# Optimization experiments

Measured on AMD Instinct MI355X. Metric: run time of the kernel, lower is better.

Reference implementation:

```python
import jax, jax.numpy as jnp
import numpy as np

BS, T, F, D_IN, NH, D_OUT = 8, 32, 128, 64, 8, 64
GAUSS_STD = 2.0


def setup_inputs() -> dict:
    key = jax.random.key(0)
    ks = jax.random.split(key, 9)
    X = jax.random.normal(ks[0], (BS, F, T, D_IN), dtype=jnp.float32)
    W_query = jax.random.normal(ks[1], (T, F, D_IN, NH, 2), dtype=jnp.float32)
    W_key = jax.random.normal(ks[2], (T, F, D_IN, NH, 2), dtype=jnp.float32)
    Wkey_ = jax.random.normal(ks[3], (T, 2, 2), dtype=jnp.float32)
    u = jax.random.normal(ks[4], (T, F, 2), dtype=jnp.float32)
    attention_center = GAUSS_STD * jax.random.normal(ks[5], (T, NH, 1), dtype=jnp.float32)
    alpha = jax.random.normal(ks[6], (T,), dtype=jnp.float32)
    # relative position features: [F, F, 2] = (delta^2, delta), tiled over T
    rel = (jnp.arange(F)[None, :] - jnp.arange(F)[:, None]).astype(jnp.float32)
    R = jnp.broadcast_to(jnp.stack([rel ** 2, rel], axis=-1)[None], (T, F, F, 2))
    W = jax.random.normal(ks[7], (T, NH * D_IN, D_OUT), dtype=jnp.float32)
    b = jax.random.normal(ks[8], (F, T, D_OUT), dtype=jnp.float32)
    return {"X": X, "W_query": W_query, "W_key": W_key, "Wkey_": Wkey_,
            "u": u, "attention_center": attention_center, "alpha": alpha,
            "R": R, "W": W, "b": b}


def reference(X, W_query, W_key, Wkey_, u, attention_center, alpha, R, W, b):
    # X: [bs, F, T, d_in] -> [bs, T, F, d_in]
    Xp = jnp.transpose(X, (0, 2, 1, 3))
    bs = Xp.shape[0]
    query = jnp.einsum('btfd,tfdhe->btfhe', Xp, W_query)  # [bs,T,F,Nh,2]
    key_t = jnp.einsum('btfd,tfdhe->btfhe', Xp, W_key)    # [bs,T,F,Nh,2]
    r_delta = jnp.einsum('tde,tfle->tfld', Wkey_, R)      # [T,F,F,2]
    centers = jnp.concatenate([jnp.ones_like(attention_center),
                               -2.0 * attention_center], axis=-1)  # [T,Nh,2]
    v = -alpha[:, None, None] * centers                   # [T,Nh,2]
    scores = (jnp.einsum('btfhe,btlhe->btfhl', query, key_t)
              + jnp.einsum('btfhe,tfle->btfhl', query, r_delta)
              + jnp.einsum('tle,btfhe->btfhl', u, key_t)
              + jnp.einsum('the,tfle->tfhl', v, r_delta)[None])  # [bs,T,F,Nh,F]
    probs = jax.nn.softmax(scores, axis=-1)
    vals = jnp.einsum('btfhl,btld->btfhd', probs, Xp)     # [bs,T,F,Nh,d_in]
    vals = vals.reshape(bs, T, F, NH * D_IN)
    out = jnp.einsum('btfd,tdo->bfto', vals, W) + b[None]  # [bs,F,T,d_out]
    return out
```

## Files before the change

### kernel.cpp

```cpp
#include <hip/hip_runtime.h>
#include <hip/hip_bf16.h>

#define NBS 8
#define NT 32
#define NF 128
#define NDIN 64
#define NNH 8
#define NDOUT 64

typedef __bf16 bf16_t;
typedef __bf16 bf16x8 __attribute__((ext_vector_type(8)));
typedef float f32x4 __attribute__((ext_vector_type(4)));
typedef float f32x2 __attribute__((ext_vector_type(2)));

__global__ __launch_bounds__(256, 4)
void qk_project_kernel(const float* __restrict__ X,
                       const float* __restrict__ Wq,
                       const float* __restrict__ Wk,
                       float* __restrict__ q_ws,
                       float* __restrict__ k_ws)
{
    __shared__ float lx[4][8][64];
    const int w = threadIdx.x >> 6, lane = threadIdx.x & 63;
    const int gw = blockIdx.x * 4 + w;
    const int t = gw >> 7, f = gw & 127;

    {
        const int b = lane >> 3, d8 = (lane & 7) << 3;
        const float* src = &X[(((size_t)b * NF + f) * NT + t) * NDIN + d8];
        const float4 v0 = *(const float4*)src;
        const float4 v1 = *(const float4*)(src + 4);
        *(float4*)&lx[w][b][d8]     = v0;
        *(float4*)&lx[w][b][d8 + 4] = v1;
    }
    __syncthreads();

    const int dq = lane >> 4, he = lane & 15;
    const float* wq = Wq + ((size_t)t * NF + f) * (NDIN * 16);
    const float* wk = Wk + ((size_t)t * NF + f) * (NDIN * 16);
    float qa[8] = {0,0,0,0,0,0,0,0}, ka[8] = {0,0,0,0,0,0,0,0};
    for (int d0 = 0; d0 < NDIN; d0 += 4) {
        const int d = d0 + dq;
        const float wqv = wq[d * 16 + he];
        const float wkv = wk[d * 16 + he];
#pragma unroll
        for (int b = 0; b < 8; ++b) {
            const float x = lx[w][b][d];
            qa[b] = fmaf(x, wqv, qa[b]);
            ka[b] = fmaf(x, wkv, ka[b]);
        }
    }
#pragma unroll
    for (int b = 0; b < 8; ++b) {
        qa[b] += __shfl_xor(qa[b], 16); qa[b] += __shfl_xor(qa[b], 32);
        ka[b] += __shfl_xor(ka[b], 16); ka[b] += __shfl_xor(ka[b], 32);
    }
#pragma unroll
    for (int bb = 0; bb < 2; ++bb) {
        const int b = dq + bb * 4;
        q_ws[(((size_t)b * NT + t) * 16 + he) * NF + f] = qa[b];
        k_ws[(((size_t)b * NT + t) * 16 + he) * NF + f] = ka[b];
    }
}

__global__ __launch_bounds__(512, 2)
void spatial_attn_kernel(const float* __restrict__ X,
                         const float* __restrict__ q_ws,
                         const float* __restrict__ k_ws,
                         const float* __restrict__ Wkey,
                         const float* __restrict__ U,
                         const float* __restrict__ AC,
                         const float* __restrict__ Alpha,
                         const float* __restrict__ Wo,
                         const float* __restrict__ Bias,
                         float* __restrict__ Out)
{
    const int blk  = blockIdx.x;
    const int b    = blk & 7;
    const int t    = blk >> 3;
    const int tid  = threadIdx.x;
    const int w    = tid >> 6;
    const int lane = tid & 63;
    const int cq   = lane & 15;
    const int rq   = lane >> 4;
    const int rt   = w;
    const int frow = 16 * rt + cq;

    __shared__ __align__(16) unsigned char smem[140288];
    bf16_t* XTs   = (bf16_t*)smem;
    float*  kvf   = (float*)(smem + 16384);
    float4 (*qf)[128] = (float4 (*)[128])(smem + 40960);
    bf16_t* WTall = (bf16_t*)(smem + 57344);
    bf16_t (*Vscr)[16][68] = (bf16_t (*)[16][68])(smem + 122880);

#pragma unroll
    for (int r = 0; r < 4; ++r) {
        const int idx = tid + r * 512;
        const int f = idx >> 4, d4 = (idx & 15) << 2;
        const float4 v = *(const float4*)&X[(((size_t)b * NF + f) * NT + t) * NDIN + d4];
        float vv[4]; vv[0] = v.x; vv[1] = v.y; vv[2] = v.z; vv[3] = v.w;
#pragma unroll
        for (int i = 0; i < 4; ++i) {
            const int d = d4 + i;
            XTs[d * 128 + (((f >> 3) ^ (d & 15)) << 3) + (f & 7)] = (bf16_t)vv[i];
        }
    }
#pragma unroll
    for (int r = 0; r < 2; ++r) {
        const int idx = tid + r * 512;
        const int hh = idx >> 7, l = idx & 127;
        const size_t qkb = ((size_t)b * NT + t) * 16;
        const float k0 = k_ws[(qkb + 2 * hh + 0) * NF + l];
        const float k1 = k_ws[(qkb + 2 * hh + 1) * NF + l];
        const float q0 = q_ws[(qkb + 2 * hh + 0) * NF + l];
        const float q1 = q_ws[(qkb + 2 * hh + 1) * NF + l];
        const float2 u01 = *(const float2*)&U[((size_t)t * NF + l) * 2];
        qf[hh][l] = make_float4(q0, q1, k0, k1);
        const int P = l >> 1, c = l & 1;
        const int base = (hh * 64 + P) * 12;
        kvf[base + 0 + c] = k0;
        kvf[base + 2 + c] = k1;
        kvf[base + 4 + c] = u01.x;
        kvf[base + 6 + c] = u01.y;
    }
#pragma unroll
    for (int rep = 0; rep < 16; ++rep) {
        const int flat = rep * 512 + tid;
        const int h = flat >> 10, f10 = flat & 1023;
        const int dd = f10 >> 4, o4 = (f10 & 15) << 2;
        const float4 v = *(const float4*)&Wo[((size_t)t * 512 + h * 64 + dd) * NDOUT + o4];
        float vv[4]; vv[0] = v.x; vv[1] = v.y; vv[2] = v.z; vv[3] = v.w;
#pragma unroll
        for (int i = 0; i < 4; ++i) {
            const int o = o4 + i;
            WTall[h * 4096 + o * 64 + (((dd >> 3) ^ (o & 7)) << 3) + (dd & 7)] = (bf16_t)vv[i];
        }
    }

    const float alpha_t = Alpha[t];
    const float wk00 = Wkey[t * 4 + 0], wk01 = Wkey[t * 4 + 1];
    const float wk10 = Wkey[t * 4 + 2], wk11 = Wkey[t * 4 + 3];

    __syncthreads();

    f32x4 oacc[4] = { {0.f,0.f,0.f,0.f}, {0.f,0.f,0.f,0.f}, {0.f,0.f,0.f,0.f}, {0.f,0.f,0.f,0.f} };

#pragma unroll 1
    for (int h = 0; h < NNH; ++h) {
        const float4 qq = qf[h][frow];
        const float q0 = qq.x, q1 = qq.y, kf0 = qq.z, kf1 = qq.w;
        const float v1 = 2.f * alpha_t * AC[t * NNH + h];
        const float c0 = (q0 - alpha_t) * wk00 + (q1 + v1) * wk10;
        const float c1 = (q0 - alpha_t) * wk01 + (q1 + v1) * wk11;

        f32x2 sc2[4][4];
        f32x2 mx2 = { -3.0e38f, -3.0e38f };
#pragma unroll
        for (int kt = 0; kt < 4; ++kt) {
#pragma unroll
            for (int j2 = 0; j2 < 4; ++j2) {
                const int P = kt * 16 + rq * 4 + j2;
                const float4 ld0 = *(const float4*)&kvf[(h * 64 + P) * 12];
                const float4 ld1 = *(const float4*)&kvf[(h * 64 + P) * 12 + 4];
                const f32x2 k0p = { ld0.x, ld0.y };
                const f32x2 k1p = { ld0.z, ld0.w };
                const f32x2 u0p = { ld1.x, ld1.y };
                const f32x2 u1p = { ld1.z, ld1.w };
                const float l0 = (float)(kt * 32 + rq * 8 + 2 * j2 - frow);
                const f32x2 delp = { l0, l0 + 1.f };
                f32x2 sv = k0p * q0 + k1p * q1 + u0p * kf0 + u1p * kf1
                         + (delp * c0 + c1) * delp;
                sc2[kt][j2] = sv;
                mx2 = __builtin_elementwise_max(mx2, sv);
            }
        }
        float rowmax = fmaxf(mx2.x, mx2.y);
        rowmax = fmaxf(rowmax, __shfl_xor(rowmax, 16));
        rowmax = fmaxf(rowmax, __shfl_xor(rowmax, 32));
        f32x2 s2 = { 0.f, 0.f };
#pragma unroll
        for (int kt = 0; kt < 4; ++kt)
#pragma unroll
            for (int j2 = 0; j2 < 4; ++j2) {
                f32x2 sv = sc2[kt][j2];
                const f32x2 e = { __expf(sv.x - rowmax), __expf(sv.y - rowmax) };
                s2 += e;
                sc2[kt][j2] = e;
            }
        float sum = s2.x + s2.y;
        sum += __shfl_xor(sum, 16);
        sum += __shfl_xor(sum, 32);
        const float rinv = 1.f / sum;

        f32x4 vacc[4] = { {0.f,0.f,0.f,0.f}, {0.f,0.f,0.f,0.f}, {0.f,0.f,0.f,0.f}, {0.f,0.f,0.f,0.f} };
#pragma unroll
        for (int kt = 0; kt < 4; ++kt) {
            bf16x8 pf;
#pragma unroll
            for (int j2 = 0; j2 < 4; ++j2) {
                const f32x2 e = sc2[kt][j2];
                pf[2 * j2 + 0] = (bf16_t)(e.x * rinv);
                pf[2 * j2 + 1] = (bf16_t)(e.y * rinv);
            }
#pragma unroll
            for (int ct = 0; ct < 4; ++ct) {
                const bf16x8 bb = *(const bf16x8*)&XTs[(ct * 16 + cq) * 128 + (((kt * 4 + rq) ^ cq) << 3)];
                vacc[ct] = __builtin_amdgcn_mfma_f32_16x16x32_bf16(pf, bb, vacc[ct], 0, 0, 0);
            }
        }
#pragma unroll
        for (int ct = 0; ct < 4; ++ct)
#pragma unroll
            for (int rr = 0; rr < 4; ++rr)
                Vscr[w][rq * 4 + rr][ct * 16 + cq] = (bf16_t)vacc[ct][rr];

#pragma unroll
        for (int kt = 0; kt < 2; ++kt) {
            const bf16x8 a = *(const bf16x8*)&Vscr[w][cq][kt * 32 + rq * 8];
#pragma unroll
            for (int ct = 0; ct < 4; ++ct) {
                const bf16x8 bw = *(const bf16x8*)&WTall[h * 4096 + (ct * 16 + cq) * 64 + (((kt * 4 + rq) ^ (cq & 7)) << 3)];
                oacc[ct] = __builtin_amdgcn_mfma_f32_16x16x32_bf16(a, bw, oacc[ct], 0, 0, 0);
            }
        }
    }

#pragma unroll
    for (int ct = 0; ct < 4; ++ct) {
#pragma unroll
        for (int rr = 0; rr < 4; ++rr) {
            const int f = 16 * rt + rq * 4 + rr;
            const int o = ct * 16 + cq;
            Out[(((size_t)b * NF + f) * NT + t) * NDOUT + o] =
                oacc[ct][rr] + Bias[((size_t)f * NT + t) * NDOUT + o];
        }
    }
}

extern "C" void kernel_launch(void* const* d_in, const int* in_sizes, int n_in,
                              void* d_out, int out_size, void* d_ws, size_t ws_size,
                              hipStream_t stream) {
    (void)in_sizes; (void)n_in; (void)ws_size; (void)out_size;
    const float* X    = (const float*)d_in[0];
    const float* Wq   = (const float*)d_in[1];
    const float* Wk   = (const float*)d_in[2];
    const float* Wkey = (const float*)d_in[3];
    const float* U    = (const float*)d_in[4];
    const float* AC   = (const float*)d_in[5];
    const float* Al   = (const float*)d_in[6];
    const float* Wo   = (const float*)d_in[8];
    const float* Bias = (const float*)d_in[9];

    float* q_ws = (float*)d_ws;
    float* k_ws = q_ws + (size_t)NBS * NT * 16 * NF;

    qk_project_kernel<<<dim3(NT * NF / 4), dim3(256), 0, stream>>>(X, Wq, Wk, q_ws, k_ws);
    spatial_attn_kernel<<<dim3(NBS * NT), dim3(512), 0, stream>>>(
        X, q_ws, k_ws, Wkey, U, AC, Al, Wo, Bias, (float*)d_out);
}
```

Before: 49.01 us.

## Double-buffer per-head output weights and deduplicate u in LDS to shrink shared memory

Shared memory per block drops from about 140KB to about 76KB. Instead of staging all eight heads of the output projection weights at once, the kernel keeps a two-slot buffer and loads the next head's weights inside the head loop. The u positional terms are stored once rather than copied for every head. The aim is to fit more blocks per CU and overlap the weight loads with compute, at the cost of a __syncthreads every iteration and global loads inside the loop.

Measured after the change: 52.24 us. +6.6%, slower.

```diff
diff --git a/kernel.cpp b/kernel.cpp
--- a/kernel.cpp
+++ b/kernel.cpp
@@ -86,12 +86,13 @@
     const int rt   = w;
     const int frow = 16 * rt + cq;
 
-    __shared__ __align__(16) unsigned char smem[140288];
+    __shared__ __align__(16) unsigned char smem[75776];
     bf16_t* XTs   = (bf16_t*)smem;
-    float*  kvf   = (float*)(smem + 16384);
-    float4 (*qf)[128] = (float4 (*)[128])(smem + 40960);
-    bf16_t* WTall = (bf16_t*)(smem + 57344);
-    bf16_t (*Vscr)[16][68] = (bf16_t (*)[16][68])(smem + 122880);
+    float*  kvh   = (float*)(smem + 16384);
+    float*  kvu   = (float*)(smem + 24576);
+    float4 (*qf)[128] = (float4 (*)[128])(smem + 25600);
+    bf16_t* WTs   = (bf16_t*)(smem + 41984);
+    bf16_t (*Vscr)[16][68] = (bf16_t (*)[16][68])(smem + 58368);
 
 #pragma unroll
     for (int r = 0; r < 4; ++r) {
@@ -114,26 +115,29 @@
         const float k1 = k_ws[(qkb + 2 * hh + 1) * NF + l];
         const float q0 = q_ws[(qkb + 2 * hh + 0) * NF + l];
         const float q1 = q_ws[(qkb + 2 * hh + 1) * NF + l];
-        const float2 u01 = *(const float2*)&U[((size_t)t * NF + l) * 2];
         qf[hh][l] = make_float4(q0, q1, k0, k1);
         const int P = l >> 1, c = l & 1;
-        const int base = (hh * 64 + P) * 12;
-        kvf[base + 0 + c] = k0;
-        kvf[base + 2 + c] = k1;
-        kvf[base + 4 + c] = u01.x;
-        kvf[base + 6 + c] = u01.y;
-    }
-#pragma unroll
-    for (int rep = 0; rep < 16; ++rep) {
-        const int flat = rep * 512 + tid;
-        const int h = flat >> 10, f10 = flat & 1023;
-        const int dd = f10 >> 4, o4 = (f10 & 15) << 2;
-        const float4 v = *(const float4*)&Wo[((size_t)t * 512 + h * 64 + dd) * NDOUT + o4];
+        const int base = (hh * 64 + P) * 4;
+        kvh[base + 0 + c] = k0;
+        kvh[base + 2 + c] = k1;
+    }
+    if (tid < 128) {
+        const int l = tid;
+        const float2 u01 = *(const float2*)&U[((size_t)t * NF + l) * 2];
+        const int P = l >> 1, c = l & 1;
+        kvu[P * 4 + 0 + c] = u01.x;
+        kvu[P * 4 + 2 + c] = u01.y;
+    }
+#pragma unroll
+    for (int r = 0; r < 2; ++r) {
+        const int idx = tid + r * 512;
+        const int dd = idx >> 4, o4 = (idx & 15) << 2;
+        const float4 v = *(const float4*)&Wo[((size_t)t * 512 + dd) * NDOUT + o4];
         float vv[4]; vv[0] = v.x; vv[1] = v.y; vv[2] = v.z; vv[3] = v.w;
 #pragma unroll
         for (int i = 0; i < 4; ++i) {
             const int o = o4 + i;
-            WTall[h * 4096 + o * 64 + (((dd >> 3) ^ (o & 7)) << 3) + (dd & 7)] = (bf16_t)vv[i];
+            WTs[o * 64 + (((dd >> 3) ^ (o & 7)) << 3) + (dd & 7)] = (bf16_t)vv[i];
         }
     }
 
@@ -147,6 +151,22 @@
 
 #pragma unroll 1
     for (int h = 0; h < NNH; ++h) {
+        if (h < 7) {
+            const int bn = ((h + 1) & 1) * 4096;
+#pragma unroll
+            for (int r = 0; r < 2; ++r) {
+                const int idx = tid + r * 512;
+                const int dd = idx >> 4, o4 = (idx & 15) << 2;
+                const float4 v = *(const float4*)&Wo[((size_t)t * 512 + (h + 1) * 64 + dd) * NDOUT + o4];
+                float vv[4]; vv[0] = v.x; vv[1] = v.y; vv[2] = v.z; vv[3] = v.w;
+#pragma unroll
+                for (int i = 0; i < 4; ++i) {
+                    const int o = o4 + i;
+                    WTs[bn + o * 64 + (((dd >> 3) ^ (o & 7)) << 3) + (dd & 7)] = (bf16_t)vv[i];
+                }
+            }
+        }
+        const int buf = (h & 1) * 4096;
         const float4 qq = qf[h][frow];
         const float q0 = qq.x, q1 = qq.y, kf0 = qq.z, kf1 = qq.w;
         const float v1 = 2.f * alpha_t * AC[t * NNH + h];
@@ -160,12 +180,12 @@
 #pragma unroll
             for (int j2 = 0; j2 < 4; ++j2) {
                 const int P = kt * 16 + rq * 4 + j2;
-                const float4 ld0 = *(const float4*)&kvf[(h * 64 + P) * 12];
-                const float4 ld1 = *(const float4*)&kvf[(h * 64 + P) * 12 + 4];
-                const f32x2 k0p = { ld0.x, ld0.y };
-                const f32x2 k1p = { ld0.z, ld0.w };
-                const f32x2 u0p = { ld1.x, ld1.y };
-                const f32x2 u1p = { ld1.z, ld1.w };
+                const float4 kp = *(const float4*)&kvh[(h * 64 + P) * 4];
+                const float4 up = *(const float4*)&kvu[P * 4];
+                const f32x2 k0p = { kp.x, kp.y };
+                const f32x2 k1p = { kp.z, kp.w };
+                const f32x2 u0p = { up.x, up.y };
+                const f32x2 u1p = { up.z, up.w };
                 const float l0 = (float)(kt * 32 + rq * 8 + 2 * j2 - frow);
                 const f32x2 delp = { l0, l0 + 1.f };
                 f32x2 sv = k0p * q0 + k1p * q1 + u0p * kf0 + u1p * kf1
@@ -219,10 +239,11 @@
             const bf16x8 a = *(const bf16x8*)&Vscr[w][cq][kt * 32 + rq * 8];
 #pragma unroll
             for (int ct = 0; ct < 4; ++ct) {
-                const bf16x8 bw = *(const bf16x8*)&WTall[h * 4096 + (ct * 16 + cq) * 64 + (((kt * 4 + rq) ^ (cq & 7)) << 3)];
+                const bf16x8 bw = *(const bf16x8*)&WTs[buf + (ct * 16 + cq) * 64 + (((kt * 4 + rq) ^ (cq & 7)) << 3)];
                 oacc[ct] = __builtin_amdgcn_mfma_f32_16x16x32_bf16(a, bw, oacc[ct], 0, 0, 0);
             }
         }
+        __syncthreads();
     }
 
 #pragma unroll
```

## Software-pipeline softmax of next head with MFMA GEMMs of current head

Applied to the files above, without the earlier changes.

Splits the per-head loop body into a probability computation (scores, softmax, bf16 packing) and the two MFMA GEMM stages. The loop is unrolled by two and computes the next head's probabilities before running the current head's GEMMs. This lets VALU/transcendental work overlap with matrix-core work. It raises register pressure, since two sets of packed probabilities stay live, which could lower occupancy or cause spills under the launch bounds.

Measured after the change: 49.15 us. Within noise of the previous version (+0.3%).

```diff
diff --git a/kernel.cpp b/kernel.cpp
--- a/kernel.cpp
+++ b/kernel.cpp
@@ -145,14 +145,12 @@
 
     f32x4 oacc[4] = { {0.f,0.f,0.f,0.f}, {0.f,0.f,0.f,0.f}, {0.f,0.f,0.f,0.f}, {0.f,0.f,0.f,0.f} };
 
-#pragma unroll 1
-    for (int h = 0; h < NNH; ++h) {
-        const float4 qq = qf[h][frow];
+    auto compute_pf = [&](const int hn, bf16x8* pf) {
+        const float4 qq = qf[hn][frow];
         const float q0 = qq.x, q1 = qq.y, kf0 = qq.z, kf1 = qq.w;
-        const float v1 = 2.f * alpha_t * AC[t * NNH + h];
+        const float v1 = 2.f * alpha_t * AC[t * NNH + hn];
         const float c0 = (q0 - alpha_t) * wk00 + (q1 + v1) * wk10;
         const float c1 = (q0 - alpha_t) * wk01 + (q1 + v1) * wk11;
-
         f32x2 sc2[4][4];
         f32x2 mx2 = { -3.0e38f, -3.0e38f };
 #pragma unroll
@@ -160,8 +158,8 @@
 #pragma unroll
             for (int j2 = 0; j2 < 4; ++j2) {
                 const int P = kt * 16 + rq * 4 + j2;
-                const float4 ld0 = *(const float4*)&kvf[(h * 64 + P) * 12];
-                const float4 ld1 = *(const float4*)&kvf[(h * 64 + P) * 12 + 4];
+                const float4 ld0 = *(const float4*)&kvf[(hn * 64 + P) * 12];
+                const float4 ld1 = *(const float4*)&kvf[(hn * 64 + P) * 12 + 4];
                 const f32x2 k0p = { ld0.x, ld0.y };
                 const f32x2 k1p = { ld0.z, ld0.w };
                 const f32x2 u0p = { ld1.x, ld1.y };
@@ -191,21 +189,25 @@
         sum += __shfl_xor(sum, 16);
         sum += __shfl_xor(sum, 32);
         const float rinv = 1.f / sum;
-
-        f32x4 vacc[4] = { {0.f,0.f,0.f,0.f}, {0.f,0.f,0.f,0.f}, {0.f,0.f,0.f,0.f}, {0.f,0.f,0.f,0.f} };
 #pragma unroll
         for (int kt = 0; kt < 4; ++kt) {
-            bf16x8 pf;
 #pragma unroll
             for (int j2 = 0; j2 < 4; ++j2) {
                 const f32x2 e = sc2[kt][j2];
-                pf[2 * j2 + 0] = (bf16_t)(e.x * rinv);
-                pf[2 * j2 + 1] = (bf16_t)(e.y * rinv);
-            }
+                pf[kt][2 * j2 + 0] = (bf16_t)(e.x * rinv);
+                pf[kt][2 * j2 + 1] = (bf16_t)(e.y * rinv);
+            }
+        }
+    };
+
+    auto gemms = [&](const int hn, const bf16x8* pf) {
+        f32x4 vacc[4] = { {0.f,0.f,0.f,0.f}, {0.f,0.f,0.f,0.f}, {0.f,0.f,0.f,0.f}, {0.f,0.f,0.f,0.f} };
+#pragma unroll
+        for (int kt = 0; kt < 4; ++kt) {
 #pragma unroll
             for (int ct = 0; ct < 4; ++ct) {
                 const bf16x8 bb = *(const bf16x8*)&XTs[(ct * 16 + cq) * 128 + (((kt * 4 + rq) ^ cq) << 3)];
-                vacc[ct] = __builtin_amdgcn_mfma_f32_16x16x32_bf16(pf, bb, vacc[ct], 0, 0, 0);
+                vacc[ct] = __builtin_amdgcn_mfma_f32_16x16x32_bf16(pf[kt], bb, vacc[ct], 0, 0, 0);
             }
         }
 #pragma unroll
@@ -213,16 +215,25 @@
 #pragma unroll
             for (int rr = 0; rr < 4; ++rr)
                 Vscr[w][rq * 4 + rr][ct * 16 + cq] = (bf16_t)vacc[ct][rr];
-
 #pragma unroll
         for (int kt = 0; kt < 2; ++kt) {
             const bf16x8 a = *(const bf16x8*)&Vscr[w][cq][kt * 32 + rq * 8];
 #pragma unroll
             for (int ct = 0; ct < 4; ++ct) {
-                const bf16x8 bw = *(const bf16x8*)&WTall[h * 4096 + (ct * 16 + cq) * 64 + (((kt * 4 + rq) ^ (cq & 7)) << 3)];
+                const bf16x8 bw = *(const bf16x8*)&WTall[hn * 4096 + (ct * 16 + cq) * 64 + (((kt * 4 + rq) ^ (cq & 7)) << 3)];
                 oacc[ct] = __builtin_amdgcn_mfma_f32_16x16x32_bf16(a, bw, oacc[ct], 0, 0, 0);
             }
         }
+    };
+
+    bf16x8 pA[4], pB[4];
+    compute_pf(0, pA);
+#pragma unroll 1
+    for (int h = 0; h < NNH; h += 2) {
+        compute_pf(h + 1, pB);
+        gemms(h, pA);
+        if (h + 2 < NNH) compute_pf(h + 2, pA);
+        gemms(h + 1, pB);
     }
 
 #pragma unroll
```
